# Kernel tuning notes

Hardware: AMD Instinct MI355X
Metric: run time of the kernel (lower is better)

## Reference

```python
import jax, jax.numpy as jnp
import numpy as np

B, S, H, A = 2, 512, 256, 128


def setup_inputs() -> dict:
    key = jax.random.key(0)
    k1, k2, k3, k4 = jax.random.split(key, 4)
    x = jax.random.normal(k1, (B, S, H), dtype=jnp.float32)
    attention_mask = jax.random.randint(k2, (B, S), 0, 2, dtype=jnp.int32)
    # xavier_normal for w_a, standard normal for query (as in torch init)
    w_a = jax.random.normal(k3, (H, A), dtype=jnp.float32) * np.sqrt(2.0 / (H + A))
    query = jax.random.normal(k4, (A,), dtype=jnp.float32)
    return {"x": x, "attention_mask": attention_mask, "w_a": w_a, "query": query}


def reference(x, attention_mask, w_a, query):
    # attention_type == 'fixed' path of SelfAttention
    b, s, h = x.shape
    tri = jnp.tril(jnp.ones((s, s), dtype=x.dtype))  # tri[i,j]=1 iff j<=i (causal)
    # values[b,i,j,h] = x[b,j,h] if j<=i else 0  (the O(S^2*H) masked broadcast)
    values = tri[None, :, :, None] * x[:, None, :, :]          # (B,S,S,H)
    key_t = jnp.tanh(jnp.einsum('bijh,ha->bija', values, w_a))  # (B,S,S,A)
    temp = jnp.einsum('a,bija->bij', query, key_t)              # (B,S,S)
    # additive softmax mask: 0 on lower triangle, -inf above diagonal
    smask = jnp.where(tri == 1, 0.0, -jnp.inf).astype(x.dtype)
    d = jax.nn.softmax(temp + smask, axis=-1)                   # (B,S,S)
    am = (attention_mask[:, :s] != 0)
    pair = (am[:, :, None] & am[:, None, :]).astype(d.dtype)    # (B,S,S)
    d = d * pair
    a = jnp.einsum('bij,bjh->bih', d, x)                        # (B,S,H)
    return (a, d)
```

## Files before the change

### kernel.cpp

```cpp
#include <hip/hip_runtime.h>
#include <math.h>

#define BB 2
#define SS 512
#define HH 256
#define AA 128
#define CH 4
#define NCH (SS / CH)
#define NBLK (BB * NCH)
#define NT 512

typedef float f4_t __attribute__((ext_vector_type(4)));

__device__ unsigned g_tick = 0;

__global__ __launch_bounds__(NT, 2)
void k_fused(const float* __restrict__ x,
             const int* __restrict__ am,
             const float* __restrict__ w_a,
             const float* __restrict__ query,
             float* __restrict__ Ews,
             float* __restrict__ Cws,
             float* __restrict__ dout,
             float* __restrict__ aout) {
    const int blk = blockIdx.x;
    const int b   = blk >> 7;
    const int c   = blk & 127;
    const int j0  = c * CH;
    const int tid = threadIdx.x;

    __shared__ float xs[CH][HH];
    __shared__ float pred[16][CH][AA];
    __shared__ float redr[CH][2];
    __shared__ float Wl[CH];
    __shared__ float Es[SS];
    __shared__ float Ws[SS];
    __shared__ float cpar[2][HH];
    __shared__ float Pinv[CH];
    __shared__ float red8[8];
    __shared__ int   amis[CH];

    {
        const float2* src = (const float2*)(x + (size_t)(b * SS + j0) * HH);
        ((float2*)&xs[0][0])[tid] = src[tid];
    }
    __syncthreads();

    const int q  = tid & 31;
    const int hs = tid >> 5;
    const int h0 = hs << 4;
    float4 acc0 = make_float4(0.f, 0.f, 0.f, 0.f);
    float4 acc1 = acc0, acc2 = acc0, acc3 = acc0;
    const float4* w4 = (const float4*)w_a;

#define ROWFMA(ACC, R)                                                          \
    {                                                                           \
        const float4 xv = *(const float4*)&xs[R][h];                            \
        ACC.x = fmaf(xv.x, wa.x, fmaf(xv.y, wb.x, fmaf(xv.z, wc.x, fmaf(xv.w, wd.x, ACC.x)))); \
        ACC.y = fmaf(xv.x, wa.y, fmaf(xv.y, wb.y, fmaf(xv.z, wc.y, fmaf(xv.w, wd.y, ACC.y)))); \
        ACC.z = fmaf(xv.x, wa.z, fmaf(xv.y, wb.z, fmaf(xv.z, wc.z, fmaf(xv.w, wd.z, ACC.z)))); \
        ACC.w = fmaf(xv.x, wa.w, fmaf(xv.y, wb.w, fmaf(xv.z, wc.w, fmaf(xv.w, wd.w, ACC.w)))); \
    }

#pragma unroll
    for (int hh = 0; hh < 16; hh += 4) {
        const int h = h0 + hh;
        const float4 wa = w4[(h + 0) * (AA / 4) + q];
        const float4 wb = w4[(h + 1) * (AA / 4) + q];
        const float4 wc = w4[(h + 2) * (AA / 4) + q];
        const float4 wd = w4[(h + 3) * (AA / 4) + q];
        ROWFMA(acc0, 0)
        ROWFMA(acc1, 1)
        ROWFMA(acc2, 2)
        ROWFMA(acc3, 3)
    }
#undef ROWFMA

    *(float4*)&pred[hs][0][q << 2] = acc0;
    *(float4*)&pred[hs][1][q << 2] = acc1;
    *(float4*)&pred[hs][2][q << 2] = acc2;
    *(float4*)&pred[hs][3][q << 2] = acc3;
    __syncthreads();

    {
        const int r = tid >> 7;
        const int a = tid & 127;
        float s = 0.f;
#pragma unroll
        for (int t = 0; t < 16; ++t) s += pred[t][r][a];
        float v = tanhf(s) * query[a];
#pragma unroll
        for (int off = 32; off; off >>= 1) v += __shfl_down(v, off, 64);
        if ((tid & 63) == 0) redr[r][(tid >> 6) & 1] = v;
    }
    if (tid < CH) amis[tid] = am[b * SS + j0 + tid];
    __syncthreads();
    if (tid < CH) {
        const float t = redr[tid][0] + redr[tid][1];
        const float e = expf(t);
        Wl[tid] = amis[tid] ? e : 0.f;
        Ews[b * SS + j0 + tid] = e;
    }
    __syncthreads();

    if (tid < HH) {
        const float cacc = fmaf(Wl[0], xs[0][tid],
                           fmaf(Wl[1], xs[1][tid],
                           fmaf(Wl[2], xs[2][tid],
                                Wl[3] * xs[3][tid])));
        Cws[(size_t)(b * NCH + c) * HH + tid] = cacc;
    }
    __syncthreads();

    if (tid == 0) {
        const unsigned old =
            __hip_atomic_fetch_add(&g_tick, 1u, __ATOMIC_RELEASE, __HIP_MEMORY_SCOPE_AGENT);
        const unsigned target = (old / NBLK + 1u) * NBLK;
        while (__hip_atomic_load(&g_tick, __ATOMIC_RELAXED, __HIP_MEMORY_SCOPE_AGENT) < target)
            __builtin_amdgcn_s_sleep(2);
        (void)__hip_atomic_load(&g_tick, __ATOMIC_ACQUIRE, __HIP_MEMORY_SCOPE_AGENT);
    }
    __syncthreads();

    {
        const float e = Ews[b * SS + tid];
        const int  m  = am[b * SS + tid];
        Es[tid] = e;
        Ws[tid] = m ? e : 0.f;
        float p = (tid <= j0) ? e : 0.f;
#pragma unroll
        for (int off = 32; off; off >>= 1) p += __shfl_down(p, off, 64);
        if ((tid & 63) == 0) red8[tid >> 6] = p;
    }
    __syncthreads();
    if (tid == 0) {
        const float P0 = ((red8[0] + red8[1]) + (red8[2] + red8[3]))
                       + ((red8[4] + red8[5]) + (red8[6] + red8[7]));
        const float P1 = P0 + Es[j0 + 1];
        const float P2 = P1 + Es[j0 + 2];
        const float P3 = P2 + Es[j0 + 3];
        Pinv[0] = 1.f / P0; Pinv[1] = 1.f / P1;
        Pinv[2] = 1.f / P2; Pinv[3] = 1.f / P3;
    }
    __syncthreads();

    {
        const int   r  = tid >> 7;
        const int   jc = (tid & 127) << 2;
        const int   i  = j0 + r;
        const float pv = Pinv[r];
        const bool  on = amis[r] != 0;
        const float4 wv = *(const float4*)&Ws[jc];
        f4_t o;
        o.x = (on && jc + 0 <= i) ? wv.x * pv : 0.f;
        o.y = (on && jc + 1 <= i) ? wv.y * pv : 0.f;
        o.z = (on && jc + 2 <= i) ? wv.z * pv : 0.f;
        o.w = (on && jc + 3 <= i) ? wv.w * pv : 0.f;
        __builtin_nontemporal_store(o, (f4_t*)&dout[(size_t)(b * SS + i) * SS + jc]);
    }

    {
        const int g = tid >> 8;
        const int h = tid & 255;
        const int nfull = c;
        const float* Cb = Cws + (size_t)b * NCH * HH + h;
        float s0 = 0.f, s1 = 0.f, s2 = 0.f, s3 = 0.f;
        int cc = g;
        for (; cc + 7 <= nfull; cc += 8) {
            s0 += Cb[(size_t)(cc + 0) * HH];
            s1 += Cb[(size_t)(cc + 2) * HH];
            s2 += Cb[(size_t)(cc + 4) * HH];
            s3 += Cb[(size_t)(cc + 6) * HH];
        }
        for (; cc < nfull; cc += 2) s0 += Cb[(size_t)cc * HH];
        cpar[g][h] = (s0 + s1) + (s2 + s3);
    }
    __syncthreads();
    if (tid < HH) {
        const int   h    = tid;
        const float base = cpar[0][h] + cpar[1][h];
        const float a0 = fmaf(Ws[j0 + 0], xs[0][h], base);
        const float a1 = fmaf(Ws[j0 + 1], xs[1][h], a0);
        const float a2 = fmaf(Ws[j0 + 2], xs[2][h], a1);
        const float a3 = fmaf(Ws[j0 + 3], xs[3][h], a2);
        const size_t arow = (size_t)(b * SS + j0) * HH + h;
        __builtin_nontemporal_store(amis[0] ? a0 * Pinv[0] : 0.f, &aout[arow + 0 * HH]);
        __builtin_nontemporal_store(amis[1] ? a1 * Pinv[1] : 0.f, &aout[arow + 1 * HH]);
        __builtin_nontemporal_store(amis[2] ? a2 * Pinv[2] : 0.f, &aout[arow + 2 * HH]);
        __builtin_nontemporal_store(amis[3] ? a3 * Pinv[3] : 0.f, &aout[arow + 3 * HH]);
    }
}

extern "C" void kernel_launch(void* const* d_in, const int* in_sizes, int n_in,
                              void* d_out, int out_size, void* d_ws, size_t ws_size,
                              hipStream_t stream) {
    const float* x     = (const float*)d_in[0];
    const int*   am    = (const int*)d_in[1];
    const float* w_a   = (const float*)d_in[2];
    const float* query = (const float*)d_in[3];

    float* a_out  = (float*)d_out;
    float* d_outp = a_out + (size_t)BB * SS * HH;

    float* Ews = (float*)d_ws;
    float* Cws = Ews + BB * SS;

    k_fused<<<NBLK, NT, 0, stream>>>(x, am, w_a, query, Ews, Cws, d_outp, a_out);
}
```

Measured before the change: 77.41 us.

## Split fused kernel at grid barrier into two kernel launches

Replaces the software grid-wide barrier (atomic counter spin) with a kernel boundary. The first kernel computes exp scores and per-chunk weighted x sums. The second kernel uses 512 blocks of 256 threads, two rows each, to write the softmax rows and the prefix-summed outputs. This removes the spin-wait and the occupancy constraint the barrier imposed, and spreads the output phase over more blocks. The cost is an extra launch and rereading x from global memory.

```diff
diff --git a/kernel.cpp b/kernel.cpp
--- a/kernel.cpp
+++ b/kernel.cpp
@@ -8,21 +8,17 @@
 #define CH 4
 #define NCH (SS / CH)
 #define NBLK (BB * NCH)
-#define NT 512
+#define NT1 512
 
 typedef float f4_t __attribute__((ext_vector_type(4)));
 
-__device__ unsigned g_tick = 0;
-
-__global__ __launch_bounds__(NT, 2)
-void k_fused(const float* __restrict__ x,
-             const int* __restrict__ am,
-             const float* __restrict__ w_a,
-             const float* __restrict__ query,
-             float* __restrict__ Ews,
-             float* __restrict__ Cws,
-             float* __restrict__ dout,
-             float* __restrict__ aout) {
+__global__ __launch_bounds__(NT1, 2)
+void k_E(const float* __restrict__ x,
+         const int* __restrict__ am,
+         const float* __restrict__ w_a,
+         const float* __restrict__ query,
+         float* __restrict__ Ews,
+         float* __restrict__ Cws) {
     const int blk = blockIdx.x;
     const int b   = blk >> 7;
     const int c   = blk & 127;
@@ -33,11 +29,6 @@
     __shared__ float pred[16][CH][AA];
     __shared__ float redr[CH][2];
     __shared__ float Wl[CH];
-    __shared__ float Es[SS];
-    __shared__ float Ws[SS];
-    __shared__ float cpar[2][HH];
-    __shared__ float Pinv[CH];
-    __shared__ float red8[8];
     __shared__ int   amis[CH];
 
     {
@@ -110,44 +101,52 @@
                                 Wl[3] * xs[3][tid])));
         Cws[(size_t)(b * NCH + c) * HH + tid] = cacc;
     }
-    __syncthreads();
-
+}
+
+__global__ __launch_bounds__(256, 4)
+void k_O(const float* __restrict__ Ews,
+         const float* __restrict__ Cws,
+         const int* __restrict__ am,
+         const float* __restrict__ x,
+         float* __restrict__ dout,
+         float* __restrict__ aout) {
+    const int blk = blockIdx.x;
+    const int b   = blk >> 8;
+    const int i0  = (blk & 255) << 1;
+    const int tid = threadIdx.x;
+    const int lane = tid & 63;
+
+    __shared__ float Es[SS];
+    __shared__ float Ws[SS];
+    __shared__ float red[4];
+    __shared__ float Pinv[2];
+    __shared__ int   amis[2];
+
+    const float e0 = Ews[b * SS + tid];
+    const float e1 = Ews[b * SS + tid + 256];
+    const int  m0  = am[b * SS + tid];
+    const int  m1  = am[b * SS + tid + 256];
+    Es[tid] = e0;             Es[tid + 256] = e1;
+    Ws[tid] = m0 ? e0 : 0.f;  Ws[tid + 256] = m1 ? e1 : 0.f;
+
+    float p = ((tid <= i0) ? e0 : 0.f) + ((tid + 256 <= i0) ? e1 : 0.f);
+#pragma unroll
+    for (int off = 32; off; off >>= 1) p += __shfl_down(p, off, 64);
+    if (lane == 0) red[tid >> 6] = p;
+    if (tid < 2) amis[tid] = am[b * SS + i0 + tid];
+    __syncthreads();
     if (tid == 0) {
-        const unsigned old =
-            __hip_atomic_fetch_add(&g_tick, 1u, __ATOMIC_RELEASE, __HIP_MEMORY_SCOPE_AGENT);
-        const unsigned target = (old / NBLK + 1u) * NBLK;
-        while (__hip_atomic_load(&g_tick, __ATOMIC_RELAXED, __HIP_MEMORY_SCOPE_AGENT) < target)
-            __builtin_amdgcn_s_sleep(2);
-        (void)__hip_atomic_load(&g_tick, __ATOMIC_ACQUIRE, __HIP_MEMORY_SCOPE_AGENT);
-    }
-    __syncthreads();
-
-    {
-        const float e = Ews[b * SS + tid];
-        const int  m  = am[b * SS + tid];
-        Es[tid] = e;
-        Ws[tid] = m ? e : 0.f;
-        float p = (tid <= j0) ? e : 0.f;
-#pragma unroll
-        for (int off = 32; off; off >>= 1) p += __shfl_down(p, off, 64);
-        if ((tid & 63) == 0) red8[tid >> 6] = p;
-    }
-    __syncthreads();
-    if (tid == 0) {
-        const float P0 = ((red8[0] + red8[1]) + (red8[2] + red8[3]))
-                       + ((red8[4] + red8[5]) + (red8[6] + red8[7]));
-        const float P1 = P0 + Es[j0 + 1];
-        const float P2 = P1 + Es[j0 + 2];
-        const float P3 = P2 + Es[j0 + 3];
-        Pinv[0] = 1.f / P0; Pinv[1] = 1.f / P1;
-        Pinv[2] = 1.f / P2; Pinv[3] = 1.f / P3;
+        const float P0 = (red[0] + red[1]) + (red[2] + red[3]);
+        const float P1 = P0 + Es[i0 + 1];
+        Pinv[0] = 1.f / P0;
+        Pinv[1] = 1.f / P1;
     }
     __syncthreads();
 
     {
         const int   r  = tid >> 7;
         const int   jc = (tid & 127) << 2;
-        const int   i  = j0 + r;
+        const int   i  = i0 + r;
         const float pv = Pinv[r];
         const bool  on = amis[r] != 0;
         const float4 wv = *(const float4*)&Ws[jc];
@@ -160,34 +159,43 @@
     }
 
     {
-        const int g = tid >> 8;
-        const int h = tid & 255;
-        const int nfull = c;
+        const int h     = tid;
+        const int nfull = i0 >> 2;
+        const int lo    = i0 & 3;
         const float* Cb = Cws + (size_t)b * NCH * HH + h;
+
         float s0 = 0.f, s1 = 0.f, s2 = 0.f, s3 = 0.f;
-        int cc = g;
-        for (; cc + 7 <= nfull; cc += 8) {
+        float s4 = 0.f, s5 = 0.f, s6 = 0.f, s7 = 0.f;
+        int cc = 0;
+        for (; cc + 8 <= nfull; cc += 8) {
             s0 += Cb[(size_t)(cc + 0) * HH];
-            s1 += Cb[(size_t)(cc + 2) * HH];
-            s2 += Cb[(size_t)(cc + 4) * HH];
-            s3 += Cb[(size_t)(cc + 6) * HH];
+            s1 += Cb[(size_t)(cc + 1) * HH];
+            s2 += Cb[(size_t)(cc + 2) * HH];
+            s3 += Cb[(size_t)(cc + 3) * HH];
+            s4 += Cb[(size_t)(cc + 4) * HH];
+            s5 += Cb[(size_t)(cc + 5) * HH];
+            s6 += Cb[(size_t)(cc + 6) * HH];
+            s7 += Cb[(size_t)(cc + 7) * HH];
         }
-        for (; cc < nfull; cc += 2) s0 += Cb[(size_t)cc * HH];
-        cpar[g][h] = (s0 + s1) + (s2 + s3);
-    }
-    __syncthreads();
-    if (tid < HH) {
-        const int   h    = tid;
-        const float base = cpar[0][h] + cpar[1][h];
-        const float a0 = fmaf(Ws[j0 + 0], xs[0][h], base);
-        const float a1 = fmaf(Ws[j0 + 1], xs[1][h], a0);
-        const float a2 = fmaf(Ws[j0 + 2], xs[2][h], a1);
-        const float a3 = fmaf(Ws[j0 + 3], xs[3][h], a2);
-        const size_t arow = (size_t)(b * SS + j0) * HH + h;
-        __builtin_nontemporal_store(amis[0] ? a0 * Pinv[0] : 0.f, &aout[arow + 0 * HH]);
-        __builtin_nontemporal_store(amis[1] ? a1 * Pinv[1] : 0.f, &aout[arow + 1 * HH]);
-        __builtin_nontemporal_store(amis[2] ? a2 * Pinv[2] : 0.f, &aout[arow + 2 * HH]);
-        __builtin_nontemporal_store(amis[3] ? a3 * Pinv[3] : 0.f, &aout[arow + 3 * HH]);
+        for (; cc < nfull; ++cc) s0 += Cb[(size_t)cc * HH];
+        float acc = ((s0 + s1) + (s2 + s3)) + ((s4 + s5) + (s6 + s7));
+
+        const int jbase = nfull << 2;
+        const float* xb = x + ((size_t)b * SS + jbase) * HH + h;
+        float av0, av1;
+        if (lo) {
+            acc = fmaf(Ws[jbase + 0], xb[0 * HH], acc);
+            acc = fmaf(Ws[jbase + 1], xb[1 * HH], acc);
+            av0 = fmaf(Ws[i0 + 0],    xb[2 * HH], acc);
+            av1 = fmaf(Ws[i0 + 1],    xb[3 * HH], av0);
+        } else {
+            av0 = fmaf(Ws[i0 + 0],    xb[0 * HH], acc);
+            av1 = fmaf(Ws[i0 + 1],    xb[1 * HH], av0);
+        }
+
+        const size_t arow = (size_t)(b * SS + i0) * HH + h;
+        __builtin_nontemporal_store(amis[0] ? av0 * Pinv[0] : 0.f, &aout[arow + 0 * HH]);
+        __builtin_nontemporal_store(amis[1] ? av1 * Pinv[1] : 0.f, &aout[arow + 1 * HH]);
     }
 }
 
@@ -205,5 +213,6 @@
     float* Ews = (float*)d_ws;
     float* Cws = Ews + BB * SS;
 
-    k_fused<<<NBLK, NT, 0, stream>>>(x, am, w_a, query, Ews, Cws, d_outp, a_out);
+    k_E<<<NBLK,       NT1, 0, stream>>>(x, am, w_a, query, Ews, Cws);
+    k_O<<<BB * SS / 2, 256, 0, stream>>>(Ews, Cws, am, x, d_outp, a_out);
 }
```

Result: faster. 72.86 us (-5.9%).
